# Optimization experiments

Measured on AMD Instinct MI355X. Metric: run time of the kernel, lower is better.

Reference implementation:

```python
import jax, jax.numpy as jnp
import numpy as np

N = 50000
E = 800000
IN_DIM = 256
HID = 128
HEADS = 2
OUT_DIM = 256
NEG_SLOPE = 0.2  # DGL GATConv default


def gat_layer(x, W, a_l, a_r, b, src, dst, num_nodes):
    """One DGL-style GATConv layer (eval mode, no dropout).
    x: [N, Fin]; W: [Fin, heads*d]; a_l, a_r: [heads, d]; b: [heads, d].
    Returns [N, heads, d].
    """
    heads, d = a_l.shape
    z = (x @ W).reshape(num_nodes, heads, d)              # [N, heads, d]
    el = jnp.einsum('nhd,hd->nh', z, a_l)                 # [N, heads]
    er = jnp.einsum('nhd,hd->nh', z, a_r)                 # [N, heads]
    e = el[src] + er[dst]                                 # [E, heads]
    e = jnp.where(e > 0, e, NEG_SLOPE * e)                # LeakyReLU
    # segment softmax over incoming edges of each dst node
    m = jax.ops.segment_max(e, dst, num_segments=num_nodes)   # [N, heads]
    ex = jnp.exp(e - m[dst])                               # [E, heads]
    s = jax.ops.segment_sum(ex, dst, num_segments=num_nodes)  # [N, heads]
    alpha = ex / s[dst]                                    # [E, heads]
    # weighted scatter-add aggregation
    msg = z[src] * alpha[:, :, None]                       # [E, heads, d]
    out = jax.ops.segment_sum(msg, dst, num_segments=num_nodes)  # [N, heads, d]
    return out + b[None, :, :]


def setup_inputs() -> dict:
    key = jax.random.key(0)
    ks = jax.random.split(key, 12)
    sc1 = 1.0 / np.sqrt(IN_DIM)
    sc2 = 1.0 / np.sqrt(HEADS * HID)
    return {
        'node_feats': jax.random.normal(ks[0], (N, IN_DIM), dtype=jnp.float32),
        'src': jax.random.randint(ks[1], (E,), 0, N, dtype=jnp.int32),
        'dst': jax.random.randint(ks[2], (E,), 0, N, dtype=jnp.int32),
        'W1': jax.random.normal(ks[3], (IN_DIM, HEADS * HID), dtype=jnp.float32) * sc1,
        'al1': jax.random.normal(ks[4], (HEADS, HID), dtype=jnp.float32) * sc1,
        'ar1': jax.random.normal(ks[5], (HEADS, HID), dtype=jnp.float32) * sc1,
        'b1': jnp.zeros((HEADS, HID), dtype=jnp.float32),
        'W2': jax.random.normal(ks[6], (HEADS * HID, OUT_DIM), dtype=jnp.float32) * sc2,
        'al2': jax.random.normal(ks[7], (1, OUT_DIM), dtype=jnp.float32) * sc2,
        'ar2': jax.random.normal(ks[8], (1, OUT_DIM), dtype=jnp.float32) * sc2,
        'b2': jnp.zeros((1, OUT_DIM), dtype=jnp.float32),
    }


def reference(node_feats, src, dst, W1, al1, ar1, b1, W2, al2, ar2, b2):
    h = gat_layer(node_feats, W1, al1, ar1, b1, src, dst, N)   # [N, heads, HID]
    h = jax.nn.relu(h.reshape(N, HEADS * HID))                 # flatten(1) + relu
    out = gat_layer(h, W2, al2, ar2, b2, src, dst, N)          # [N, 1, OUT_DIM]
    return out[:, 0, :]                                        # squeeze(1)
```

## Files before the change

kernel.cpp:

```cpp
#include <hip/hip_runtime.h>
#include <hip/hip_fp16.h>
#include <math.h>


typedef _Float16 half8 __attribute__((ext_vector_type(8)));
typedef float floatx4 __attribute__((ext_vector_type(4)));

__device__ __forceinline__ float rl_f(float x, int i) {
  return __int_as_float(__builtin_amdgcn_readlane(__float_as_int(x), i));
}
__device__ __forceinline__ float cvt_h(unsigned u) {
  return __half2float(__ushort_as_half((unsigned short)(u & 0xffffu)));
}
__device__ __forceinline__ unsigned pk2(float a, float b) {
  return (unsigned)__half_as_ushort(__float2half_rn(a)) |
         ((unsigned)__half_as_ushort(__float2half_rn(b)) << 16);
}

__global__ __launch_bounds__(256) void zero_f4(float4* __restrict__ p, int n4) {
  int i = blockIdx.x * 256 + threadIdx.x;
  if (i < n4) p[i] = make_float4(0.f, 0.f, 0.f, 0.f);
}

__global__ __launch_bounds__(256) void cvt_half(const float4* __restrict__ in,
                                                uint2* __restrict__ outh, int n4) {
  int i = blockIdx.x * 256 + threadIdx.x;
  if (i < n4) {
    float4 v = in[i];
    uint2 o;
    o.x = pk2(v.x, v.y);
    o.y = pk2(v.z, v.w);
    outh[i] = o;
  }
}

__global__ __launch_bounds__(256) void transpose_w(const float* __restrict__ W,
                                                   unsigned short* __restrict__ Wt) {
  int k = blockIdx.x, n = threadIdx.x;
  Wt[n * 256 + k] = __half_as_ushort(__float2half_rn(W[k * 256 + n]));
}

__global__ __launch_bounds__(256) void hist_dst(const int* __restrict__ dst,
                                                int* __restrict__ counts, int E) {
  int i = blockIdx.x * 256 + threadIdx.x;
  if (i < E) atomicAdd(&counts[dst[i]], 1);
}

__global__ __launch_bounds__(256) void scan_block(const int* __restrict__ counts,
                                                  int* __restrict__ offsets,
                                                  int* __restrict__ bsum, int Nn) {
  __shared__ int sm[256];
  int t = threadIdx.x;
  int i = blockIdx.x * 256 + t;
  int v = (i < Nn) ? counts[i] : 0;
  sm[t] = v;
  __syncthreads();
  for (int off = 1; off < 256; off <<= 1) {
    int x = (t >= off) ? sm[t - off] : 0;
    __syncthreads();
    sm[t] += x;
    __syncthreads();
  }
  if (i < Nn) offsets[i] = sm[t] - v;
  if (t == 255) bsum[blockIdx.x] = sm[255];
}

__global__ __launch_bounds__(256) void scan_bsum(int* __restrict__ bsum,
                                                 int* __restrict__ bofs, int B) {
  __shared__ int sm[256];
  int t = threadIdx.x;
  int v = (t < B) ? bsum[t] : 0;
  sm[t] = v;
  __syncthreads();
  for (int off = 1; off < 256; off <<= 1) {
    int x = (t >= off) ? sm[t - off] : 0;
    __syncthreads();
    sm[t] += x;
    __syncthreads();
  }
  if (t < B) bofs[t] = sm[t] - v;
}

__global__ __launch_bounds__(256) void scan_add(int* __restrict__ offsets,
                                                const int* __restrict__ bofs,
                                                int* __restrict__ cursor, int Nn) {
  int i = blockIdx.x * 256 + threadIdx.x;
  if (i < Nn) {
    int o = offsets[i] + bofs[i >> 8];
    offsets[i] = o;
    cursor[i] = o;
  }
}

__global__ __launch_bounds__(256) void scatter_edges(const int* __restrict__ src,
                                                     const int* __restrict__ dst,
                                                     int* __restrict__ cursor,
                                                     int* __restrict__ esrc, int E) {
  int i = blockIdx.x * 256 + threadIdx.x;
  if (i < E) {
    int pos = atomicAdd(&cursor[dst[i]], 1);
    esrc[pos] = src[i];
  }
}

__global__ __launch_bounds__(256) void gemm_mfma(const unsigned short* __restrict__ A,
                                                 const unsigned short* __restrict__ Wt,
                                                 unsigned short* __restrict__ C, int M) {
  const int tid = threadIdx.x;
  const int wv = tid >> 6, lane = tid & 63;
  const int ln = lane & 15, kg = lane >> 4;

  half8 bf[8][4];
#pragma unroll
  for (int kb = 0; kb < 8; kb++)
#pragma unroll
    for (int t = 0; t < 4; t++)
      bf[kb][t] = *(const half8*)(Wt + (size_t)((4 * wv + t) * 16 + ln) * 256 +
                                  kb * 32 + kg * 8);

  const int nchunk = (M + 31) >> 5;
  for (int c = blockIdx.x; c < nchunk; c += gridDim.x) {
    const int m0 = c << 5;

    floatx4 acc[2][4];
#pragma unroll
    for (int mt = 0; mt < 2; mt++)
#pragma unroll
      for (int t = 0; t < 4; t++) acc[mt][t] = (floatx4)0.f;

    half8 af[2][8];
    const int row0 = m0 + ln, row1 = m0 + 16 + ln;
    const unsigned short* ap0 = A + (size_t)((row0 < M) ? row0 : (M - 1)) * 256 + kg * 8;
    const unsigned short* ap1 = A + (size_t)((row1 < M) ? row1 : (M - 1)) * 256 + kg * 8;
#pragma unroll
    for (int kb = 0; kb < 8; kb++) {
      af[0][kb] = *(const half8*)(ap0 + kb * 32);
      af[1][kb] = *(const half8*)(ap1 + kb * 32);
    }

#pragma unroll
    for (int kb = 0; kb < 8; kb++)
#pragma unroll
      for (int mt = 0; mt < 2; mt++)
#pragma unroll
        for (int t = 0; t < 4; t++)
          acc[mt][t] = __builtin_amdgcn_mfma_f32_16x16x32_f16(bf[kb][t], af[mt][kb],
                                                              acc[mt][t], 0, 0, 0);

#pragma unroll
    for (int mt = 0; mt < 2; mt++) {
      const int row = m0 + mt * 16 + ln;
      if (row < M) {
        unsigned short* cp = C + (size_t)row * 256 + (4 * wv) * 16 + kg * 4;
#pragma unroll
        for (int t = 0; t < 4; t++) {
          uint2 o;
          o.x = pk2(acc[mt][t].x, acc[mt][t].y);
          o.y = pk2(acc[mt][t].z, acc[mt][t].w);
          *(uint2*)(cp + t * 16) = o;
        }
      }
    }
  }
}

__global__ __launch_bounds__(256) void attn_dots(const unsigned short* __restrict__ z,
                                                 const float* __restrict__ al,
                                                 const float* __restrict__ ar,
                                                 float* __restrict__ el,
                                                 float* __restrict__ er,
                                                 int NH, int hshift, int d) {
  int wid = (blockIdx.x * 256 + threadIdx.x) >> 6;
  int lane = threadIdx.x & 63;
  if (wid >= NH) return;
  int h = wid & ((1 << hshift) - 1);
  int n = wid >> hshift;
  const unsigned short* zp = z + (size_t)n * 256 + h * d;
  const float* alp = al + h * d;
  const float* arp = ar + h * d;
  float pl = 0.f, pr = 0.f;
  for (int j0 = lane * 2; j0 < d; j0 += 128) {
    unsigned u = *(const unsigned*)(zp + j0);
    float f0 = cvt_h(u), f1 = cvt_h(u >> 16);
    pl += f0 * alp[j0] + f1 * alp[j0 + 1];
    pr += f0 * arp[j0] + f1 * arp[j0 + 1];
  }
#pragma unroll
  for (int o = 32; o > 0; o >>= 1) {
    pl += __shfl_down(pl, o);
    pr += __shfl_down(pr, o);
  }
  if (lane == 0) { el[wid] = pl; er[wid] = pr; }
}

template <int HS, int DS, int RELU, int OUTH>
__global__ __launch_bounds__(256) void node_aggregate(const unsigned short* __restrict__ z,
                                                      const float* __restrict__ el,
                                                      const float* __restrict__ er,
                                                      const int* __restrict__ esrc,
                                                      const int* __restrict__ offsets,
                                                      const int* __restrict__ counts,
                                                      const float* __restrict__ bias,
                                                      void* __restrict__ out, int Nn) {
  int n = (blockIdx.x * 256 + threadIdx.x) >> 6;
  int lane = threadIdx.x & 63;
  if (n >= Nn) return;
  const int beg = offsets[n];
  const int deg = counts[n];
  float ern0, ern1 = 0.f;
  if (HS) {
    float2 e = ((const float2*)er)[n];
    ern0 = e.x; ern1 = e.y;
  } else {
    ern0 = er[n];
  }
  const int head = HS ? ((lane << 2) >> DS) : 0;

  float m0 = -INFINITY, m1 = -INFINITY;
  float s0p = 0.f, s1p = 0.f;
  float4 acc = make_float4(0.f, 0.f, 0.f, 0.f);

  for (int base = 0; base < deg; base += 64) {
    const int cnt = min(64, deg - base);
    int sn = 0;
    float v0 = -INFINITY, v1 = -INFINITY;
    if (lane < cnt) {
      sn = esrc[beg + base + lane];
      if (HS) {
        float2 elv = ((const float2*)el)[sn];
        v0 = elv.x + ern0; v0 = (v0 > 0.f) ? v0 : 0.2f * v0;
        v1 = elv.y + ern1; v1 = (v1 > 0.f) ? v1 : 0.2f * v1;
      } else {
        v0 = el[sn] + ern0; v0 = (v0 > 0.f) ? v0 : 0.2f * v0;
      }
    }
    float cm0 = v0, cm1 = v1;
#pragma unroll
    for (int o = 32; o > 0; o >>= 1) {
      cm0 = fmaxf(cm0, __shfl_xor(cm0, o));
      if (HS) cm1 = fmaxf(cm1, __shfl_xor(cm1, o));
    }
    const float nm0 = fmaxf(m0, cm0);
    const float sc0 = __expf(m0 - nm0);
    float nm1 = nm0, sc1 = sc0;
    if (HS) { nm1 = fmaxf(m1, cm1); sc1 = __expf(m1 - nm1); }
    s0p = s0p * sc0;
    const float myex0 = __expf(v0 - nm0);
    s0p += myex0;
    float myex1 = 0.f;
    if (HS) { s1p = s1p * sc1; myex1 = __expf(v1 - nm1); s1p += myex1; }
    const float sch = (HS && head) ? sc1 : sc0;
    acc.x *= sch; acc.y *= sch; acc.z *= sch; acc.w *= sch;
    m0 = nm0; m1 = nm1;

    int i = 0;
    for (; i + 8 <= cnt; i += 8) {
      int s_[8];
      float e_[8];
      uint2 zv[8];
#pragma unroll
      for (int j = 0; j < 8; j++) {
        s_[j] = __builtin_amdgcn_readlane(sn, i + j);
        float e0 = rl_f(myex0, i + j);
        if (HS) {
          float e1 = rl_f(myex1, i + j);
          e_[j] = head ? e1 : e0;
        } else {
          e_[j] = e0;
        }
      }
#pragma unroll
      for (int j = 0; j < 8; j++)
        zv[j] = ((const uint2*)(z + ((size_t)s_[j] << 8)))[lane];
#pragma unroll
      for (int j = 0; j < 8; j++) {
        acc.x += cvt_h(zv[j].x) * e_[j];
        acc.y += cvt_h(zv[j].x >> 16) * e_[j];
        acc.z += cvt_h(zv[j].y) * e_[j];
        acc.w += cvt_h(zv[j].y >> 16) * e_[j];
      }
    }
    for (; i < cnt; i++) {
      int si = __builtin_amdgcn_readlane(sn, i);
      float e = rl_f(myex0, i);
      if (HS) {
        float e1 = rl_f(myex1, i);
        if (head) e = e1;
      }
      uint2 zv = ((const uint2*)(z + ((size_t)si << 8)))[lane];
      acc.x += cvt_h(zv.x) * e;
      acc.y += cvt_h(zv.x >> 16) * e;
      acc.z += cvt_h(zv.y) * e;
      acc.w += cvt_h(zv.y >> 16) * e;
    }
  }

#pragma unroll
  for (int o = 32; o > 0; o >>= 1) {
    s0p += __shfl_xor(s0p, o);
    if (HS) s1p += __shfl_xor(s1p, o);
  }
  const float s = (HS && head) ? s1p : s0p;
  float4 bb = ((const float4*)bias)[lane];
  float4 v;
  if (deg > 0) {
    float inv = 1.f / s;
    v = make_float4(acc.x * inv + bb.x, acc.y * inv + bb.y,
                    acc.z * inv + bb.z, acc.w * inv + bb.w);
  } else {
    v = bb;
  }
  if (RELU) {
    v.x = fmaxf(v.x, 0.f); v.y = fmaxf(v.y, 0.f);
    v.z = fmaxf(v.z, 0.f); v.w = fmaxf(v.w, 0.f);
  }
  if (OUTH) {
    uint2 o;
    o.x = pk2(v.x, v.y);
    o.y = pk2(v.z, v.w);
    ((uint2*)out)[((size_t)n << 6) + lane] = o;
  } else {
    ((float4*)out)[((size_t)n << 6) + lane] = v;
  }
}

extern "C" void kernel_launch(void* const* d_in, const int* in_sizes, int n_in,
                              void* d_out, int out_size, void* d_ws, size_t ws_size,
                              hipStream_t stream) {
  const float* x   = (const float*)d_in[0];
  const int*   src = (const int*)d_in[1];
  const int*   dst = (const int*)d_in[2];
  const float* W1  = (const float*)d_in[3];
  const float* al1 = (const float*)d_in[4];
  const float* ar1 = (const float*)d_in[5];
  const float* b1  = (const float*)d_in[6];
  const float* W2  = (const float*)d_in[7];
  const float* al2 = (const float*)d_in[8];
  const float* ar2 = (const float*)d_in[9];
  const float* b2  = (const float*)d_in[10];
  float* out = (float*)d_out;
  (void)n_in; (void)out_size; (void)ws_size;

  const int Nn = in_sizes[0] / 256;
  const int Ee = in_sizes[1];
  const int F = 256;
  const int NB = (Nn + 255) / 256;

  unsigned short* z   = (unsigned short*)d_ws;
  unsigned short* xh  = z + (size_t)Nn * F;
  unsigned short* w1t = xh + (size_t)Nn * F;
  unsigned short* w2t = w1t + 65536;
  int*   esrc   = (int*)(w2t + 65536);
  int*   counts = esrc + Ee;
  int*   offs   = counts + Nn;
  int*   cursor = offs + Nn;
  int*   bsum   = cursor + Nn;
  int*   bofs   = bsum + 256;
  float* el1p   = (float*)(bofs + 256);
  float* er1p   = el1p + (size_t)Nn * 2;
  float* el2p   = er1p + (size_t)Nn * 2;
  float* er2p   = el2p + Nn;

  dim3 blk(256);

  cvt_half<<<(Nn * 64 + 255) / 256, blk, 0, stream>>>((const float4*)x, (uint2*)xh, Nn * 64);
  transpose_w<<<256, blk, 0, stream>>>(W1, w1t);
  transpose_w<<<256, blk, 0, stream>>>(W2, w2t);

  zero_f4<<<(Nn / 4 + 255) / 256, blk, 0, stream>>>((float4*)counts, Nn / 4);
  hist_dst<<<(Ee + 255) / 256, blk, 0, stream>>>(dst, counts, Ee);
  scan_block<<<NB, blk, 0, stream>>>(counts, offs, bsum, Nn);
  scan_bsum<<<1, blk, 0, stream>>>(bsum, bofs, NB);
  scan_add<<<NB, blk, 0, stream>>>(offs, bofs, cursor, Nn);
  scatter_edges<<<(Ee + 255) / 256, blk, 0, stream>>>(src, dst, cursor, esrc, Ee);

  const int gemm_grid = 512;

  gemm_mfma<<<gemm_grid, blk, 0, stream>>>(xh, w1t, z, Nn);
  attn_dots<<<(Nn * 2 + 3) / 4, blk, 0, stream>>>(z, al1, ar1, el1p, er1p, Nn * 2, 1, 128);
  node_aggregate<1, 7, 1, 1><<<(Nn + 3) / 4, blk, 0, stream>>>(z, el1p, er1p, esrc, offs,
                                                               counts, b1, xh, Nn);

  gemm_mfma<<<gemm_grid, blk, 0, stream>>>(xh, w2t, z, Nn);
  attn_dots<<<(Nn + 3) / 4, blk, 0, stream>>>(z, al2, ar2, el2p, er2p, Nn, 0, 256);
  node_aggregate<0, 8, 0, 0><<<(Nn + 3) / 4, blk, 0, stream>>>(z, el2p, er2p, esrc, offs,
                                                               counts, b2, out, Nn);
}
```

Measured before the change: 421.8 us.

## Fuse attention dot products into GEMM epilogue and drop softmax max pass

Computes el/er inside the MFMA GEMM epilogue from the fp32 accumulators. It uses cross-lane shuffles plus atomics into zeroed buffers, which removes the separate attn_dots kernels and their re-read of z. The GEMM now uses 16-row chunks with an occupancy hint of 2 blocks per CU. The aggregation kernel drops the online max-rescaling and exponentiates the raw leaky-relu scores directly. This saves the wave reductions and rescale multiplies, but risks overflow for large logits. The two weight transposes are merged into one launch, and a single zero kernel clears the counts and the el/er accumulators.

```diff
diff --git a/kernel.cpp b/kernel.cpp
--- a/kernel.cpp
+++ b/kernel.cpp
@@ -9,12 +9,18 @@
 __device__ __forceinline__ float rl_f(float x, int i) {
   return __int_as_float(__builtin_amdgcn_readlane(__float_as_int(x), i));
 }
-__device__ __forceinline__ float cvt_h(unsigned u) {
-  return __half2float(__ushort_as_half((unsigned short)(u & 0xffffu)));
-}
 __device__ __forceinline__ unsigned pk2(float a, float b) {
   return (unsigned)__half_as_ushort(__float2half_rn(a)) |
          ((unsigned)__half_as_ushort(__float2half_rn(b)) << 16);
+}
+
+__device__ __forceinline__ void fma_row(float4& acc, uint2 zv, float e) {
+  union { uint2 u; __half h[4]; } w;
+  w.u = zv;
+  acc.x = fmaf(__half2float(w.h[0]), e, acc.x);
+  acc.y = fmaf(__half2float(w.h[1]), e, acc.y);
+  acc.z = fmaf(__half2float(w.h[2]), e, acc.z);
+  acc.w = fmaf(__half2float(w.h[3]), e, acc.w);
 }
 
 __global__ __launch_bounds__(256) void zero_f4(float4* __restrict__ p, int n4) {
@@ -34,9 +40,14 @@
   }
 }
 
-__global__ __launch_bounds__(256) void transpose_w(const float* __restrict__ W,
-                                                   unsigned short* __restrict__ Wt) {
-  int k = blockIdx.x, n = threadIdx.x;
+__global__ __launch_bounds__(256) void transpose_w2(const float* __restrict__ W1,
+                                                    const float* __restrict__ W2,
+                                                    unsigned short* __restrict__ w1t,
+                                                    unsigned short* __restrict__ w2t) {
+  int b = blockIdx.x;
+  const float* W = (b < 256) ? W1 : W2;
+  unsigned short* Wt = (b < 256) ? w1t : w2t;
+  int k = b & 255, n = threadIdx.x;
   Wt[n * 256 + k] = __half_as_ushort(__float2half_rn(W[k * 256 + n]));
 }
 
@@ -103,9 +114,14 @@
   }
 }
 
-__global__ __launch_bounds__(256) void gemm_mfma(const unsigned short* __restrict__ A,
-                                                 const unsigned short* __restrict__ Wt,
-                                                 unsigned short* __restrict__ C, int M) {
+template <int HS>
+__global__ __launch_bounds__(256, 2) void gemm_mfma(const unsigned short* __restrict__ A,
+                                                    const unsigned short* __restrict__ Wt,
+                                                    unsigned short* __restrict__ C,
+                                                    const float* __restrict__ al,
+                                                    const float* __restrict__ ar,
+                                                    float* __restrict__ el,
+                                                    float* __restrict__ er, int M) {
   const int tid = threadIdx.x;
   const int wv = tid >> 6, lane = tid & 63;
   const int ln = lane & 15, kg = lane >> 4;
@@ -118,82 +134,62 @@
       bf[kb][t] = *(const half8*)(Wt + (size_t)((4 * wv + t) * 16 + ln) * 256 +
                                   kb * 32 + kg * 8);
 
-  const int nchunk = (M + 31) >> 5;
+  const int cb = wv * 64 + kg * 4;
+  float4 av[4], rv[4];
+#pragma unroll
+  for (int t = 0; t < 4; t++) {
+    av[t] = *(const float4*)(al + cb + t * 16);
+    rv[t] = *(const float4*)(ar + cb + t * 16);
+  }
+
+  const int nchunk = (M + 15) >> 4;
   for (int c = blockIdx.x; c < nchunk; c += gridDim.x) {
-    const int m0 = c << 5;
-
-    floatx4 acc[2][4];
-#pragma unroll
-    for (int mt = 0; mt < 2; mt++)
-#pragma unroll
-      for (int t = 0; t < 4; t++) acc[mt][t] = (floatx4)0.f;
-
-    half8 af[2][8];
-    const int row0 = m0 + ln, row1 = m0 + 16 + ln;
-    const unsigned short* ap0 = A + (size_t)((row0 < M) ? row0 : (M - 1)) * 256 + kg * 8;
-    const unsigned short* ap1 = A + (size_t)((row1 < M) ? row1 : (M - 1)) * 256 + kg * 8;
-#pragma unroll
-    for (int kb = 0; kb < 8; kb++) {
-      af[0][kb] = *(const half8*)(ap0 + kb * 32);
-      af[1][kb] = *(const half8*)(ap1 + kb * 32);
-    }
+    const int m0 = c << 4;
+    const int row = m0 + ln;
+    const unsigned short* ap = A + (size_t)((row < M) ? row : (M - 1)) * 256 + kg * 8;
+
+    half8 af[8];
+#pragma unroll
+    for (int kb = 0; kb < 8; kb++) af[kb] = *(const half8*)(ap + kb * 32);
+
+    floatx4 acc[4];
+#pragma unroll
+    for (int t = 0; t < 4; t++) acc[t] = (floatx4)0.f;
 
 #pragma unroll
     for (int kb = 0; kb < 8; kb++)
 #pragma unroll
-      for (int mt = 0; mt < 2; mt++)
-#pragma unroll
-        for (int t = 0; t < 4; t++)
-          acc[mt][t] = __builtin_amdgcn_mfma_f32_16x16x32_f16(bf[kb][t], af[mt][kb],
-                                                              acc[mt][t], 0, 0, 0);
-
-#pragma unroll
-    for (int mt = 0; mt < 2; mt++) {
-      const int row = m0 + mt * 16 + ln;
-      if (row < M) {
-        unsigned short* cp = C + (size_t)row * 256 + (4 * wv) * 16 + kg * 4;
-#pragma unroll
-        for (int t = 0; t < 4; t++) {
-          uint2 o;
-          o.x = pk2(acc[mt][t].x, acc[mt][t].y);
-          o.y = pk2(acc[mt][t].z, acc[mt][t].w);
-          *(uint2*)(cp + t * 16) = o;
-        }
-      }
-    }
-  }
-}
-
-__global__ __launch_bounds__(256) void attn_dots(const unsigned short* __restrict__ z,
-                                                 const float* __restrict__ al,
-                                                 const float* __restrict__ ar,
-                                                 float* __restrict__ el,
-                                                 float* __restrict__ er,
-                                                 int NH, int hshift, int d) {
-  int wid = (blockIdx.x * 256 + threadIdx.x) >> 6;
-  int lane = threadIdx.x & 63;
-  if (wid >= NH) return;
-  int h = wid & ((1 << hshift) - 1);
-  int n = wid >> hshift;
-  const unsigned short* zp = z + (size_t)n * 256 + h * d;
-  const float* alp = al + h * d;
-  const float* arp = ar + h * d;
-  float pl = 0.f, pr = 0.f;
-  for (int j0 = lane * 2; j0 < d; j0 += 128) {
-    unsigned u = *(const unsigned*)(zp + j0);
-    float f0 = cvt_h(u), f1 = cvt_h(u >> 16);
-    pl += f0 * alp[j0] + f1 * alp[j0 + 1];
-    pr += f0 * arp[j0] + f1 * arp[j0 + 1];
-  }
-#pragma unroll
-  for (int o = 32; o > 0; o >>= 1) {
-    pl += __shfl_down(pl, o);
-    pr += __shfl_down(pr, o);
-  }
-  if (lane == 0) { el[wid] = pl; er[wid] = pr; }
-}
-
-template <int HS, int DS, int RELU, int OUTH>
+      for (int t = 0; t < 4; t++)
+        acc[t] = __builtin_amdgcn_mfma_f32_16x16x32_f16(bf[kb][t], af[kb], acc[t], 0, 0, 0);
+
+    float pl = 0.f, pr = 0.f;
+#pragma unroll
+    for (int t = 0; t < 4; t++) {
+      pl += acc[t].x * av[t].x + acc[t].y * av[t].y + acc[t].z * av[t].z + acc[t].w * av[t].w;
+      pr += acc[t].x * rv[t].x + acc[t].y * rv[t].y + acc[t].z * rv[t].z + acc[t].w * rv[t].w;
+    }
+    pl += __shfl_xor(pl, 16); pl += __shfl_xor(pl, 32);
+    pr += __shfl_xor(pr, 16); pr += __shfl_xor(pr, 32);
+
+    if (row < M) {
+      if (lane < 16) {
+        const int idx = HS ? (row * 2 + (wv >> 1)) : row;
+        atomicAdd(&el[idx], pl);
+        atomicAdd(&er[idx], pr);
+      }
+      unsigned short* cp = C + (size_t)row * 256 + wv * 64 + kg * 4;
+#pragma unroll
+      for (int t = 0; t < 4; t++) {
+        uint2 o;
+        o.x = pk2(acc[t].x, acc[t].y);
+        o.y = pk2(acc[t].z, acc[t].w);
+        *(uint2*)(cp + t * 16) = o;
+      }
+    }
+  }
+}
+
+template <int HS, int RELU, int OUTH>
 __global__ __launch_bounds__(256) void node_aggregate(const unsigned short* __restrict__ z,
                                                       const float* __restrict__ el,
                                                       const float* __restrict__ er,
@@ -214,44 +210,31 @@
   } else {
     ern0 = er[n];
   }
-  const int head = HS ? ((lane << 2) >> DS) : 0;
-
-  float m0 = -INFINITY, m1 = -INFINITY;
-  float s0p = 0.f, s1p = 0.f;
+  const int head = HS ? (lane >> 5) : 0;
+
+  float s0 = 0.f, s1 = 0.f;
   float4 acc = make_float4(0.f, 0.f, 0.f, 0.f);
+  const uint2* zp = (const uint2*)z;
 
   for (int base = 0; base < deg; base += 64) {
     const int cnt = min(64, deg - base);
     int sn = 0;
-    float v0 = -INFINITY, v1 = -INFINITY;
+    float myex0 = 0.f, myex1 = 0.f;
     if (lane < cnt) {
       sn = esrc[beg + base + lane];
       if (HS) {
         float2 elv = ((const float2*)el)[sn];
-        v0 = elv.x + ern0; v0 = (v0 > 0.f) ? v0 : 0.2f * v0;
-        v1 = elv.y + ern1; v1 = (v1 > 0.f) ? v1 : 0.2f * v1;
+        float v0 = elv.x + ern0; v0 = (v0 > 0.f) ? v0 : 0.2f * v0;
+        float v1 = elv.y + ern1; v1 = (v1 > 0.f) ? v1 : 0.2f * v1;
+        myex0 = __expf(v0);
+        myex1 = __expf(v1);
       } else {
-        v0 = el[sn] + ern0; v0 = (v0 > 0.f) ? v0 : 0.2f * v0;
-      }
-    }
-    float cm0 = v0, cm1 = v1;
-#pragma unroll
-    for (int o = 32; o > 0; o >>= 1) {
-      cm0 = fmaxf(cm0, __shfl_xor(cm0, o));
-      if (HS) cm1 = fmaxf(cm1, __shfl_xor(cm1, o));
-    }
-    const float nm0 = fmaxf(m0, cm0);
-    const float sc0 = __expf(m0 - nm0);
-    float nm1 = nm0, sc1 = sc0;
-    if (HS) { nm1 = fmaxf(m1, cm1); sc1 = __expf(m1 - nm1); }
-    s0p = s0p * sc0;
-    const float myex0 = __expf(v0 - nm0);
-    s0p += myex0;
-    float myex1 = 0.f;
-    if (HS) { s1p = s1p * sc1; myex1 = __expf(v1 - nm1); s1p += myex1; }
-    const float sch = (HS && head) ? sc1 : sc0;
-    acc.x *= sch; acc.y *= sch; acc.z *= sch; acc.w *= sch;
-    m0 = nm0; m1 = nm1;
+        float v0 = el[sn] + ern0; v0 = (v0 > 0.f) ? v0 : 0.2f * v0;
+        myex0 = __expf(v0);
+      }
+      s0 += myex0;
+      s1 += myex1;
+    }
 
     int i = 0;
     for (; i + 8 <= cnt; i += 8) {
@@ -270,15 +253,9 @@
         }
       }
 #pragma unroll
-      for (int j = 0; j < 8; j++)
-        zv[j] = ((const uint2*)(z + ((size_t)s_[j] << 8)))[lane];
-#pragma unroll
-      for (int j = 0; j < 8; j++) {
-        acc.x += cvt_h(zv[j].x) * e_[j];
-        acc.y += cvt_h(zv[j].x >> 16) * e_[j];
-        acc.z += cvt_h(zv[j].y) * e_[j];
-        acc.w += cvt_h(zv[j].y >> 16) * e_[j];
-      }
+      for (int j = 0; j < 8; j++) zv[j] = zp[((size_t)s_[j] << 6) + lane];
+#pragma unroll
+      for (int j = 0; j < 8; j++) fma_row(acc, zv[j], e_[j]);
     }
     for (; i < cnt; i++) {
       int si = __builtin_amdgcn_readlane(sn, i);
@@ -287,20 +264,17 @@
         float e1 = rl_f(myex1, i);
         if (head) e = e1;
       }
-      uint2 zv = ((const uint2*)(z + ((size_t)si << 8)))[lane];
-      acc.x += cvt_h(zv.x) * e;
-      acc.y += cvt_h(zv.x >> 16) * e;
-      acc.z += cvt_h(zv.y) * e;
-      acc.w += cvt_h(zv.y >> 16) * e;
+      uint2 zv = zp[((size_t)si << 6) + lane];
+      fma_row(acc, zv, e);
     }
   }
 
 #pragma unroll
   for (int o = 32; o > 0; o >>= 1) {
-    s0p += __shfl_xor(s0p, o);
-    if (HS) s1p += __shfl_xor(s1p, o);
-  }
-  const float s = (HS && head) ? s1p : s0p;
+    s0 += __shfl_xor(s0, o);
+    if (HS) s1 += __shfl_xor(s1, o);
+  }
+  const float s = (HS && head) ? s1 : s0;
   float4 bb = ((const float4*)bias)[lane];
   float4 v;
   if (deg > 0) {
@@ -364,10 +338,11 @@
   dim3 blk(256);
 
   cvt_half<<<(Nn * 64 + 255) / 256, blk, 0, stream>>>((const float4*)x, (uint2*)xh, Nn * 64);
-  transpose_w<<<256, blk, 0, stream>>>(W1, w1t);
-  transpose_w<<<256, blk, 0, stream>>>(W2, w2t);
-
-  zero_f4<<<(Nn / 4 + 255) / 256, blk, 0, stream>>>((float4*)counts, Nn / 4);
+  transpose_w2<<<512, blk, 0, stream>>>(W1, W2, w1t, w2t);
+
+  const int zn4 = (9 * Nn + 512) / 4;
+  zero_f4<<<(zn4 + 255) / 256, blk, 0, stream>>>((float4*)counts, zn4);
+
   hist_dst<<<(Ee + 255) / 256, blk, 0, stream>>>(dst, counts, Ee);
   scan_block<<<NB, blk, 0, stream>>>(counts, offs, bsum, Nn);
   scan_bsum<<<1, blk, 0, stream>>>(bsum, bofs, NB);
@@ -376,13 +351,11 @@
 
   const int gemm_grid = 512;
 
-  gemm_mfma<<<gemm_grid, blk, 0, stream>>>(xh, w1t, z, Nn);
-  attn_dots<<<(Nn * 2 + 3) / 4, blk, 0, stream>>>(z, al1, ar1, el1p, er1p, Nn * 2, 1, 128);
-  node_aggregate<1, 7, 1, 1><<<(Nn + 3) / 4, blk, 0, stream>>>(z, el1p, er1p, esrc, offs,
-                                                               counts, b1, xh, Nn);
-
-  gemm_mfma<<<gemm_grid, blk, 0, stream>>>(xh, w2t, z, Nn);
-  attn_dots<<<(Nn + 3) / 4, blk, 0, stream>>>(z, al2, ar2, el2p, er2p, Nn, 0, 256);
-  node_aggregate<0, 8, 0, 0><<<(Nn + 3) / 4, blk, 0, stream>>>(z, el2p, er2p, esrc, offs,
-                                                               counts, b2, out, Nn);
-}
+  gemm_mfma<1><<<gemm_grid, blk, 0, stream>>>(xh, w1t, z, al1, ar1, el1p, er1p, Nn);
+  node_aggregate<1, 1, 1><<<(Nn + 3) / 4, blk, 0, stream>>>(z, el1p, er1p, esrc, offs,
+                                                            counts, b1, xh, Nn);
+
+  gemm_mfma<0><<<gemm_grid, blk, 0, stream>>>(xh, w2t, z, al2, ar2, el2p, er2p, Nn);
+  node_aggregate<0, 0, 0><<<(Nn + 3) / 4, blk, 0, stream>>>(z, el2p, er2p, esrc, offs,
+                                                            counts, b2, out, Nn);
+}
```

Measured after the change: 380.5 us. 1.11x faster.
